# Performance work log

Hardware: AMD Instinct MI355X
Metric: run time of the kernel (lower is better)

The kernel has to match this reference:

```python
import jax, jax.numpy as jnp
import numpy as np

B, N, NUM_CLASSES, M, K = 64, 900, 128, 64, 8
COST_CLASS = 1.0
COST_BBOX = 5.0
INF = jnp.float32(1e9)


def _lsa(cost):
    """Jonker-Volgenant shortest-augmenting-path linear sum assignment.
    cost: [M, N] with M <= N (rows = targets, cols = predictions).
    Returns assigned column (prediction index) per row (target), shape [M] int32.
    Equivalent pairing to scipy.optimize.linear_sum_assignment."""
    Mr, Nc = cost.shape
    # column 0 is a dummy column (1-indexed columns, as in the classic formulation)
    a = jnp.concatenate([jnp.zeros((Mr, 1), cost.dtype), cost], axis=1)

    def assign_row(carry, i1):
        u, v, p = carry  # u:[M+1] row potentials, v:[N+1] col potentials, p:[N+1] row assigned to col (0=free)
        p = p.at[0].set(i1)
        init = (u, v, p,
                jnp.full(Nc + 1, INF, cost.dtype),   # minv
                jnp.zeros(Nc + 1, bool),             # used
                jnp.zeros(Nc + 1, jnp.int32),        # way (parent col)
                jnp.int32(0))                        # j0

        def cond(st):
            return st[2][st[6]] != 0

        def body(st):
            u, v, p, minv, used, way, j0 = st
            used = used.at[j0].set(True)
            i0 = p[j0]
            cur = a[i0 - 1] - u[i0] - v              # reduced costs of row i0 over all cols
            better = (cur < minv) & (~used)
            minv = jnp.where(better, cur, minv)
            way = jnp.where(better, j0, way)
            masked = jnp.where(used, INF, minv)
            j1 = jnp.argmin(masked).astype(jnp.int32)
            delta = masked[j1]
            u = u.at[p].add(jnp.where(used, delta, jnp.float32(0.0)))
            v = v - jnp.where(used, delta, jnp.float32(0.0))
            minv = jnp.where(used, minv, minv - delta)
            return (u, v, p, minv, used, way, j1)

        u, v, p, minv, used, way, j0 = jax.lax.while_loop(cond, body, init)

        def bt_body(st):  # backtrack the augmenting path
            p_, jj = st
            j1 = way[jj]
            return p_.at[jj].set(p_[j1]), j1

        p, _ = jax.lax.while_loop(lambda st: st[1] != 0, bt_body, (p, j0))
        return (u, v, p), None

    u0 = jnp.zeros(Mr + 1, cost.dtype)
    v0 = jnp.zeros(Nc + 1, cost.dtype)
    p0 = jnp.zeros(Nc + 1, jnp.int32)
    (u, v, p), _ = jax.lax.scan(assign_row, (u0, v0, p0),
                                jnp.arange(1, Mr + 1, dtype=jnp.int32))
    rows = p[1:]                                     # [N]: 1-indexed target row per pred col, 0 = free
    res = jnp.zeros(Mr, jnp.int32)
    res = res.at[jnp.where(rows > 0, rows - 1, Mr)].set(
        jnp.arange(Nc, dtype=jnp.int32), mode='drop')
    return res


def setup_inputs() -> dict:
    key = jax.random.key(0)
    k1, k2, k3, k4 = jax.random.split(key, 4)
    return {
        'class_logits': jax.random.normal(k1, (B, N, NUM_CLASSES), jnp.float32),
        'corners': jax.random.normal(k2, (B, N, K, 3), jnp.float32),
        'tgt_labels': jax.random.randint(k3, (B, M), 0, NUM_CLASSES, jnp.int32),
        'boxes': jax.random.normal(k4, (B, M, 7), jnp.float32),
    }


def reference(class_logits, corners, tgt_labels, boxes):
    probs = jax.nn.softmax(class_logits, axis=-1)                        # [B,N,C]
    idx = jnp.broadcast_to(tgt_labels[:, None, :], (B, N, M))
    class_cost = -jnp.take_along_axis(probs, idx, axis=2)               # [B,N,M]
    centers = corners.mean(axis=2)                                       # [B,N,3]
    diff = centers[:, :, None, :] - boxes[:, None, :, :3]                # [B,N,M,3]
    box_cost = jnp.sqrt(jnp.sum(diff * diff, axis=-1))                   # cdist, p=2
    C = COST_CLASS * class_cost + COST_BBOX * box_cost                   # [B,N,M]
    pred_idx = jax.vmap(_lsa)(jnp.swapaxes(C, 1, 2))                     # [B,M]: pred assigned to each target
    tgt_idx = jnp.broadcast_to(jnp.arange(M, dtype=jnp.int32), pred_idx.shape)
    return C, pred_idx, tgt_idx
```

## Files before the change

kernel.cpp:

```cpp
#include <hip/hip_runtime.h>
#include <math.h>

#define Bv   64
#define Nv   900
#define Mv   64
#define NCls 128
#define NCOLS (Nv + 1)
#define KREG 15
#define INFV 1000000000.0f
#define BIGV 1.0e18f

#define SEL15(arr, kidx, dst) do {            \
    int _s = arr[0];                          \
    _Pragma("unroll")                         \
    for (int _kk = 1; _kk < KREG; _kk++)      \
        _s = ((kidx) == _kk) ? arr[_kk] : _s; \
    (dst) = _s;                               \
} while (0)

#define SELTREE15(arr, kidx, dst) do {                      \
    int _a0 = ((kidx) & 1) ? arr[1]  : arr[0];              \
    int _a1 = ((kidx) & 1) ? arr[3]  : arr[2];              \
    int _a2 = ((kidx) & 1) ? arr[5]  : arr[4];              \
    int _a3 = ((kidx) & 1) ? arr[7]  : arr[6];              \
    int _a4 = ((kidx) & 1) ? arr[9]  : arr[8];              \
    int _a5 = ((kidx) & 1) ? arr[11] : arr[10];             \
    int _a6 = ((kidx) & 1) ? arr[13] : arr[12];             \
    int _a7 = arr[14];              \
    int _b0 = ((kidx) & 2) ? _a1 : _a0;                     \
    int _b1 = ((kidx) & 2) ? _a3 : _a2;                     \
    int _b2 = ((kidx) & 2) ? _a5 : _a4;                     \
    int _b3 = ((kidx) & 2) ? _a7 : _a6;                     \
    int _c0 = ((kidx) & 4) ? _b1 : _b0;                     \
    int _c1 = ((kidx) & 4) ? _b3 : _b2;                     \
    (dst)   = ((kidx) & 8) ? _c1 : _c0;                     \
} while (0)

#define SET15(arr, kidx, val) do {            \
    _Pragma("unroll")                         \
    for (int _kk = 0; _kk < KREG; _kk++)      \
        if ((kidx) == _kk) arr[_kk] = (val);  \
} while (0)

__device__ __forceinline__ unsigned f2s(float f) {
    unsigned x = __float_as_uint(f);
    return x ^ ((unsigned)((int)x >> 31) | 0x80000000u);
}
__device__ __forceinline__ float s2f(unsigned s) {
    unsigned x = ((int)s < 0) ? (s ^ 0x80000000u) : ~s;
    return __uint_as_float(x);
}

__device__ __forceinline__ void wave_min_pair(unsigned& hi, unsigned& lo) {
#define DPP_STEP(ctrl, rmask)                                                   \
    {                                                                           \
        unsigned ohi = (unsigned)__builtin_amdgcn_update_dpp(                   \
            (int)hi, (int)hi, ctrl, rmask, 0xf, false);                         \
        unsigned olo = (unsigned)__builtin_amdgcn_update_dpp(                   \
            (int)lo, (int)lo, ctrl, rmask, 0xf, false);                         \
        bool take = (ohi < hi) || (ohi == hi && olo < lo);                      \
        hi = take ? ohi : hi;                                                   \
        lo = take ? olo : lo;                                                   \
    }
    DPP_STEP(0x111, 0xf)
    DPP_STEP(0x112, 0xf)
    DPP_STEP(0x114, 0xf)
    DPP_STEP(0x118, 0xf)
    DPP_STEP(0x142, 0xa)
    DPP_STEP(0x143, 0xc)
#undef DPP_STEP
    hi = (unsigned)__builtin_amdgcn_readlane((int)hi, 63);
    lo = (unsigned)__builtin_amdgcn_readlane((int)lo, 63);
}

__device__ __forceinline__ float wave_sum_f32(float x) {
#define SSTEP(ctrl, rmask)                                                \
    {                                                                     \
        int o = __builtin_amdgcn_update_dpp(0, __float_as_int(x),         \
                                            ctrl, rmask, 0xf, false);     \
        x += __int_as_float(o);                                           \
    }
    SSTEP(0x111, 0xf) SSTEP(0x112, 0xf) SSTEP(0x114, 0xf) SSTEP(0x118, 0xf)
    SSTEP(0x142, 0xa) SSTEP(0x143, 0xc)
#undef SSTEP
    return __int_as_float(__builtin_amdgcn_readlane(__float_as_int(x), 63));
}

__global__ __launch_bounds__(256) void cost_kernel(
    const float* __restrict__ logits,
    const float* __restrict__ corners,
    const int*   __restrict__ labels,
    const float* __restrict__ boxes,
    float*       __restrict__ C)
{
    const int b = blockIdx.y;
    const int n = blockIdx.x * 4 + (threadIdx.x >> 6);
    const int t = threadIdx.x & 63;
    const long bn = (long)b * Nv + n;

    const float2 l2 = ((const float2*)(logits + bn * NCls))[t];
    const float* cp = corners + bn * 24;
    float cx = 0.f, cy = 0.f, cz = 0.f;
    if (t < 8) { cx = cp[3 * t]; cy = cp[3 * t + 1]; cz = cp[3 * t + 2]; }
    const int    lbl = labels[b * Mv + t];
    const float* bx  = boxes + ((long)b * Mv + t) * 7;
    const float bx0 = bx[0], bx1 = bx[1], bx2 = bx[2];

    float e0 = expf(l2.x), e1 = expf(l2.y);
    float s  = wave_sum_f32(e0 + e1);

    cx = wave_sum_f32(cx) * 0.125f;
    cy = wave_sum_f32(cy) * 0.125f;
    cz = wave_sum_f32(cz) * 0.125f;

    float p0 = __shfl(e0, lbl >> 1, 64);
    float p1 = __shfl(e1, lbl >> 1, 64);
    float pm = ((lbl & 1) ? p1 : p0) / s;

    float dx = cx - bx0, dy = cy - bx1, dz = cz - bx2;
    C[bn * Mv + t] = 5.0f * sqrtf(dx * dx + dy * dy + dz * dz) - pm;
}

__global__ __launch_bounds__(64) void lsa_kernel(
    const float* __restrict__ C,
    float* __restrict__ outPred, float* __restrict__ outTgt)
{
    const int b = blockIdx.x;
    const int t = threadIdx.x;
    const float* cb = C + (size_t)b * Nv * Mv;

    float mv0 = INFV, mv1 = INFV, mv2 = INFV, mv3 = INFV;
    int   mj0 = 0,    mj1 = 0,    mj2 = 0,    mj3 = 0;
    #pragma unroll 9
    for (int n = 0; n < 225; ++n) {
        float c0 = cb[(size_t)(n      ) * Mv + t];
        float c1 = cb[(size_t)(n + 225) * Mv + t];
        float c2 = cb[(size_t)(n + 450) * Mv + t];
        float c3 = cb[(size_t)(n + 675) * Mv + t];
        if (c0 < mv0) { mv0 = c0; mj0 = n;       }
        if (c1 < mv1) { mv1 = c1; mj1 = n + 225; }
        if (c2 < mv2) { mv2 = c2; mj2 = n + 450; }
        if (c3 < mv3) { mv3 = c3; mj3 = n + 675; }
    }
    float rowmin = mv0; int rown = mj0;
    if (mv1 < rowmin) { rowmin = mv1; rown = mj1; }
    if (mv2 < rowmin) { rowmin = mv2; rown = mj2; }
    if (mv3 < rowmin) { rowmin = mv3; rown = mj3; }

    float u_reg = rowmin;
    const int jcol = rown + 1;

    bool isdup = false;
    #pragma unroll
    for (int s = 1; s < 64; ++s) {
        int oj = __shfl(jcol, (t + 64 - s) & 63, 64);
        isdup |= (oj == jcol) && (s <= t);
    }
    unsigned long long pending = __ballot(isdup);

    int   p_reg[KREG], way_reg[KREG];
    float v_reg[KREG], minv[KREG], crow[KREG];
    #pragma unroll
    for (int k = 0; k < KREG; k++) { p_reg[k] = 0; way_reg[k] = 0; v_reg[k] = 0.f; }

    int rowcol = isdup ? 0 : jcol;

    #pragma unroll 8
    for (int i = 0; i < 64; ++i) {
        int jb = __shfl(jcol, i, 64);
        if (!((pending >> i) & 1ull) && t == (jb & 63))
            SET15(p_reg, jb >> 6, i + 1);
    }

    while (pending) {
        const int i1v = __ffsll(pending);
        pending &= pending - 1;

        unsigned usedMask = (t == 0) ? 1u : 0u;
        unsigned long long rowMask = 0;
        #pragma unroll
        for (int k = 0; k < KREG; k++) minv[k] = INFV;

        int j0 = 0;
        int i0 = i1v;

        #pragma unroll
        for (int k = 0; k < KREG; k++) {
            int j = t + (k << 6);
            crow[k] = (j >= 1 && j < NCOLS)
                      ? cb[(((size_t)(j - 1)) << 6) + (i0 - 1)] : BIGV;
        }

        while (true) {
            rowMask |= 1ull << (i0 - 1);
            const int sl = __builtin_amdgcn_readfirstlane(i0 - 1);
            const float u_i0 = __int_as_float(
                __builtin_amdgcn_readlane(__float_as_int(u_reg), sl));

            float bv0 = INFV, bv1 = INFV, bv2 = INFV;
            int   bk0 = 0,    bk1 = 5,    bk2 = 10;
            #pragma unroll
            for (int k = 0; k < 5; k++) {
                float cur = (crow[k] - u_i0) - v_reg[k];
                if (cur < minv[k]) { minv[k] = cur; way_reg[k] = j0; }
                if (minv[k] < bv0) { bv0 = minv[k]; bk0 = k; }
            }
            #pragma unroll
            for (int k = 5; k < 10; k++) {
                float cur = (crow[k] - u_i0) - v_reg[k];
                if (cur < minv[k]) { minv[k] = cur; way_reg[k] = j0; }
                if (minv[k] < bv1) { bv1 = minv[k]; bk1 = k; }
            }
            #pragma unroll
            for (int k = 10; k < KREG; k++) {
                float cur = (crow[k] - u_i0) - v_reg[k];
                if (cur < minv[k]) { minv[k] = cur; way_reg[k] = j0; }
                if (minv[k] < bv2) { bv2 = minv[k]; bk2 = k; }
            }
            if (bv1 < bv0) { bv0 = bv1; bk0 = bk1; }
            if (bv2 < bv0) { bv0 = bv2; bk0 = bk2; }

            int pcand; SELTREE15(p_reg, bk0, pcand);

            unsigned hi = f2s(bv0);
            unsigned lo = ((unsigned)(t + (bk0 << 6)) << 7) | (unsigned)pcand;
            wave_min_pair(hi, lo);
            const float delta = s2f(hi);
            const int   j1    = (int)(lo >> 7);
            const int   inext = (int)(lo & 0x7fu);

            const int k1 = j1 >> 6, l1 = j1 & 63;

            const bool newbit = (t == l1);
            unsigned newUsed = usedMask | (newbit ? (1u << k1) : 0u);
            if (inext != 0) {
                const int src = inext - 1;
                #pragma unroll
                for (int k = 0; k < KREG; k++) {
                    int j = t + (k << 6);
                    bool valid = (j >= 1 && j < NCOLS) && !((newUsed >> k) & 1u);
                    crow[k] = valid
                              ? cb[(((size_t)(j - 1)) << 6) + src] : BIGV;
                }
            }

            if ((rowMask >> t) & 1ull) u_reg += delta;
            #pragma unroll
            for (int k = 0; k < KREG; k++) {
                bool used  = (usedMask >> k) & 1u;
                bool isnew = newbit && (k == k1);
                v_reg[k] = used ? v_reg[k] - delta : v_reg[k];
                float mupd = used ? minv[k] : minv[k] - delta;
                minv[k] = isnew ? INFV : mupd;
            }
            usedMask = newUsed;

            j0 = j1;
            i0 = inext;
            if (i0 == 0) break;
        }

        while (j0 != 0) {
            const int k0 = j0 >> 6, l0 = j0 & 63;
            int wtmp; SEL15(way_reg, k0, wtmp);
            const int jprev = __shfl(wtmp, l0, 64);
            int pv;
            if (jprev == 0) {
                pv = i1v;
            } else {
                int ptmp2; SEL15(p_reg, jprev >> 6, ptmp2);
                pv = __shfl(ptmp2, jprev & 63, 64);
            }
            if (t == l0) SET15(p_reg, k0, pv);
            if (t == pv - 1) rowcol = j0;
            j0 = jprev;
        }
    }

    outPred[b * Mv + t] = (float)(rowcol - 1);
    outTgt[b * Mv + t]  = (float)t;
}

extern "C" void kernel_launch(void* const* d_in, const int* in_sizes, int n_in,
                              void* d_out, int out_size, void* d_ws, size_t ws_size,
                              hipStream_t stream)
{
    (void)in_sizes; (void)n_in; (void)out_size; (void)d_ws; (void)ws_size;

    const float* logits  = (const float*)d_in[0];
    const float* corners = (const float*)d_in[1];
    const int*   labels  = (const int*)  d_in[2];
    const float* boxes   = (const float*)d_in[3];

    float* out  = (float*)d_out;
    float* Cc   = out;
    float* pred = out + (size_t)Bv * Nv * Mv;
    float* tgt  = pred + (size_t)Bv * Mv;

    cost_kernel<<<dim3(225, Bv), 256, 0, stream>>>(logits, corners, labels, boxes, Cc);
    lsa_kernel<<<Bv, 64, 0, stream>>>(Cc, pred, tgt);
}
```

Before: 236.5 us.

## Add auction-style augmenting row reduction phase before shortest-path augmentation

```diff
diff --git a/kernel.cpp b/kernel.cpp
--- a/kernel.cpp
+++ b/kernel.cpp
@@ -7,6 +7,7 @@
 #define NCls 128
 #define NCOLS (Nv + 1)
 #define KREG 15
+#define ARR_CAP 160
 #define INFV 1000000000.0f
 #define BIGV 1.0e18f
 
@@ -172,6 +173,65 @@
             SET15(p_reg, jb >> 6, i + 1);
     }
 
+    int steps = 0;
+    while (pending && steps < ARR_CAP) {
+        ++steps;
+        const int iv = __ffsll(pending);
+        pending &= pending - 1;
+
+        #pragma unroll
+        for (int k = 0; k < KREG; k++) {
+            int j = t + (k << 6);
+            crow[k] = (j >= 1 && j < NCOLS)
+                      ? cb[(((size_t)(j - 1)) << 6) + (iv - 1)] : BIGV;
+        }
+
+        float m1l = BIGV; int k1l = 0;
+        #pragma unroll
+        for (int k = 0; k < KREG; k++) {
+            float r = crow[k] - v_reg[k];
+            minv[k] = r;
+            if (r < m1l) { m1l = r; k1l = k; }
+        }
+        int pc1; SELTREE15(p_reg, k1l, pc1);
+        unsigned h1 = f2s(m1l);
+        unsigned o1 = ((unsigned)(t + (k1l << 6)) << 7) | (unsigned)pc1;
+        wave_min_pair(h1, o1);
+        const float min1 = s2f(h1);
+        const int   j1   = (int)(o1 >> 7);
+        const int   own1 = (int)(o1 & 0x7fu);
+        const int   k1   = j1 >> 6, l1 = j1 & 63;
+
+        float m2l = BIGV; int k2l = 0;
+        #pragma unroll
+        for (int k = 0; k < KREG; k++) {
+            float r = ((t == l1) && (k == k1)) ? BIGV : minv[k];
+            if (r < m2l) { m2l = r; k2l = k; }
+        }
+        int pc2; SELTREE15(p_reg, k2l, pc2);
+        unsigned h2 = f2s(m2l);
+        unsigned o2 = ((unsigned)(t + (k2l << 6)) << 7) | (unsigned)pc2;
+        wave_min_pair(h2, o2);
+        const float min2 = s2f(h2);
+        const int   j2   = (int)(o2 >> 7);
+        const int   own2 = (int)(o2 & 0x7fu);
+
+        const bool strict = (min1 < min2);
+        const int jt   = (strict || own1 == 0) ? j1 : j2;
+        const int ownt = (strict || own1 == 0) ? own1 : own2;
+
+        if (t == iv - 1) u_reg = min2;
+        if (strict && t == l1) v_reg[k1] -= (min2 - min1);
+
+        if (ownt != 0) {
+            pending |= 1ull << (ownt - 1);
+            if (t == ownt - 1) rowcol = 0;
+        }
+        const int kt = jt >> 6, lt = jt & 63;
+        if (t == lt) SET15(p_reg, kt, iv);
+        if (t == iv - 1) rowcol = jt;
+    }
+
     while (pending) {
         const int i1v = __ffsll(pending);
         pending &= pending - 1;
@@ -221,7 +281,6 @@
             if (bv2 < bv0) { bv0 = bv2; bk0 = bk2; }
 
             int pcand; SELTREE15(p_reg, bk0, pcand);
-
             unsigned hi = f2s(bv0);
             unsigned lo = ((unsigned)(t + (bk0 << 6)) << 7) | (unsigned)pcand;
             wave_min_pair(hi, lo);
```

Result: slower. 384.1 us (+62.4%).
